# Performance work log

Hardware: AMD Instinct MI355X
Metric: run time of the kernel (lower is better)

Reference implementation:

```python
import jax, jax.numpy as jnp
import numpy as np

D_MODEL = 1024
SEQ = 2048
BATCH = 2
D_STATE = 16
D_CONV = 4
EXPAND = 2
D_INNER = EXPAND * D_MODEL          # 2048
DT_RANK = (D_MODEL + 15) // 16      # 64 (mamba_ssm default ceil(d_model/16))


def setup_inputs() -> dict:
    key = jax.random.key(0)
    keys = iter(jax.random.split(key, 40))

    def w(shape, scale):
        return jax.random.normal(next(keys), shape, jnp.float32) * scale

    inp = {"x": jax.random.normal(next(keys), (BATCH, SEQ, D_MODEL), jnp.float32)}
    inp["gamma"] = jnp.ones((D_MODEL,), jnp.float32)
    inp["beta"] = jnp.zeros((D_MODEL,), jnp.float32)
    for p in ("fw", "bw"):
        inp[f"{p}_in_w"] = w((2 * D_INNER, D_MODEL), 0.02)
        inp[f"{p}_conv_w"] = w((D_INNER, D_CONV), 0.2)
        inp[f"{p}_conv_b"] = jnp.zeros((D_INNER,), jnp.float32)
        inp[f"{p}_xproj_w"] = w((DT_RANK + 2 * D_STATE, D_INNER), 0.02)
        inp[f"{p}_dt_w"] = w((D_INNER, DT_RANK), 0.1)
        inp[f"{p}_dt_b"] = w((D_INNER,), 0.1)
        # S4D-real init: A = -[1..d_state], as in mamba_ssm
        inp[f"{p}_A_log"] = jnp.log(
            jnp.tile(jnp.arange(1, D_STATE + 1, dtype=jnp.float32), (D_INNER, 1))
        )
        inp[f"{p}_D"] = jnp.ones((D_INNER,), jnp.float32)
        inp[f"{p}_out_w"] = w((D_MODEL, D_INNER), 0.02)
    return inp


def _mamba(x, in_w, conv_w, conv_b, xproj_w, dt_w, dt_b, A_log, D_skip, out_w):
    """Single Mamba block: in_proj -> causal depthwise conv -> silu -> SSM -> gate -> out_proj."""
    B, L, _ = x.shape
    xz = x @ in_w.T                       # (B, L, 2*D_INNER)
    u, z = jnp.split(xz, 2, axis=-1)      # each (B, L, D_INNER)

    # causal depthwise conv over time
    uc = jnp.transpose(u, (0, 2, 1))      # (B, D_INNER, L)
    kernel = conv_w[:, None, :]           # (D_INNER, 1, D_CONV)
    uc = jax.lax.conv_general_dilated(
        uc, kernel, window_strides=(1,), padding=[(D_CONV - 1, 0)],
        dimension_numbers=("NCH", "OIH", "NCH"), feature_group_count=D_INNER)
    u = jax.nn.silu(jnp.transpose(uc, (0, 2, 1)) + conv_b)  # (B, L, D_INNER)

    # input-dependent dt, B, C
    dbc = u @ xproj_w.T                   # (B, L, DT_RANK + 2*D_STATE)
    dt = jax.nn.softplus(dbc[..., :DT_RANK] @ dt_w.T + dt_b)   # (B, L, D_INNER)
    Bc = dbc[..., DT_RANK:DT_RANK + D_STATE]                   # (B, L, D_STATE)
    Cc = dbc[..., DT_RANK + D_STATE:]                          # (B, L, D_STATE)
    A = -jnp.exp(A_log)                   # (D_INNER, D_STATE)

    def step(h, ins):
        dt_t, B_t, C_t, u_t = ins         # (B,Di) (B,Ds) (B,Ds) (B,Di)
        dA = jnp.exp(dt_t[..., None] * A)                      # (B, Di, Ds)
        h = dA * h + dt_t[..., None] * B_t[:, None, :] * u_t[..., None]
        y = jnp.einsum("bds,bs->bd", h, C_t)
        return h, y

    h0 = jnp.zeros((B, D_INNER, D_STATE), x.dtype)
    xs = (jnp.moveaxis(dt, 1, 0), jnp.moveaxis(Bc, 1, 0),
          jnp.moveaxis(Cc, 1, 0), jnp.moveaxis(u, 1, 0))
    _, ys = jax.lax.scan(step, h0, xs)    # ys: (L, B, D_INNER)
    y = jnp.moveaxis(ys, 0, 1) + u * D_skip
    y = y * jax.nn.silu(z)
    return y @ out_w.T                    # (B, L, D_MODEL)


def _layernorm(x, gamma, beta, eps=1e-5):
    mu = jnp.mean(x, axis=-1, keepdims=True)
    var = jnp.mean(jnp.square(x - mu), axis=-1, keepdims=True)
    return (x - mu) * jax.lax.rsqrt(var + eps) * gamma + beta


def reference(x, gamma, beta,
              fw_in_w, fw_conv_w, fw_conv_b, fw_xproj_w, fw_dt_w, fw_dt_b,
              fw_A_log, fw_D, fw_out_w,
              bw_in_w, bw_conv_w, bw_conv_b, bw_xproj_w, bw_dt_w, bw_dt_b,
              bw_A_log, bw_D, bw_out_w):
    # norm_first=True path; dropout=0 (eval)
    working = _layernorm(x, gamma, beta)
    f_out = _mamba(working, fw_in_w, fw_conv_w, fw_conv_b, fw_xproj_w,
                   fw_dt_w, fw_dt_b, fw_A_log, fw_D, fw_out_w)
    b_in = jnp.flip(working, axis=1)
    b_out = _mamba(b_in, bw_in_w, bw_conv_w, bw_conv_b, bw_xproj_w,
                   bw_dt_w, bw_dt_b, bw_A_log, bw_D, bw_out_w)
    b_out = jnp.flip(b_out, axis=1)
    return x + 0.5 * (f_out + b_out)
```

## Files before the change

### kernel.cpp

```cpp
#include <hip/hip_runtime.h>
#include <hip/hip_bf16.h>
#include <math.h>

#define B_    2
#define L_    2048
#define DM_   1024
#define DI_   2048
#define DS_   16
#define DTR_  64
#define NXZ_  4096
#define NDBC_ 96

#define NSEG   64
#define SEGLEN 32
#define CT     16
#define KS_    8
#define KO_    2

#define LOG2E 1.4426950408889634f

typedef __attribute__((ext_vector_type(8))) short bf16x8;
typedef __attribute__((ext_vector_type(4))) float f32x4;

__device__ __forceinline__ void gload_lds16(const void* g, void* l) {
    __builtin_amdgcn_global_load_lds(
        (const __attribute__((address_space(1))) void*)g,
        (__attribute__((address_space(3))) void*)l,
        16, 0, 0);
}

__device__ __forceinline__ float bf2f(short s) {
    union { unsigned u; float f; } x;
    x.u = ((unsigned)(unsigned short)s) << 16;
    return x.f;
}

__global__ __launch_bounds__(256)
void ln_kernel(const float* __restrict__ x,
               const float* __restrict__ gamma,
               const float* __restrict__ beta,
               __hip_bfloat16* __restrict__ out)
{
    int row = blockIdx.x;
    int t = threadIdx.x;
    const float* xr = x + (size_t)row * DM_;
    float4 v = ((const float4*)xr)[t];
    float s  = v.x + v.y + v.z + v.w;
    float ss = v.x*v.x + v.y*v.y + v.z*v.z + v.w*v.w;
    #pragma unroll
    for (int m = 1; m < 64; m <<= 1) {
        s  += __shfl_xor(s,  m, 64);
        ss += __shfl_xor(ss, m, 64);
    }
    __shared__ float as_[4], ass_[4];
    int w = t >> 6;
    if ((t & 63) == 0) { as_[w] = s; ass_[w] = ss; }
    __syncthreads();
    s  = as_[0] + as_[1] + as_[2] + as_[3];
    ss = ass_[0] + ass_[1] + ass_[2] + ass_[3];
    float mu  = s * (1.0f / DM_);
    float var = ss * (1.0f / DM_) - mu * mu;
    float inv = rsqrtf(var + 1e-5f);
    float4 g  = ((const float4*)gamma)[t];
    float4 bt = ((const float4*)beta)[t];
    __hip_bfloat16 ob[4];
    ob[0] = __float2bfloat16((v.x - mu) * inv * g.x + bt.x);
    ob[1] = __float2bfloat16((v.y - mu) * inv * g.y + bt.y);
    ob[2] = __float2bfloat16((v.z - mu) * inv * g.z + bt.z);
    ob[3] = __float2bfloat16((v.w - mu) * inv * g.w + bt.w);
    ((ushort4*)(out + (size_t)row * DM_))[t] = *(const ushort4*)ob;
}

__global__ __launch_bounds__(256)
void cvt_all(const float* __restrict__ inw_f, const float* __restrict__ inw_b,
             const float* __restrict__ ow_f,  const float* __restrict__ ow_b,
             const float* __restrict__ xp_f,  const float* __restrict__ xp_b,
             const float* __restrict__ dw_f,  const float* __restrict__ dw_b,
             __hip_bfloat16* __restrict__ win,
             __hip_bfloat16* __restrict__ wocat,
             __hip_bfloat16* __restrict__ xpw,
             __hip_bfloat16* __restrict__ dtw)
{
    const int N_WIN = 2 * NXZ_ * DM_;
    const int N_WO  = DM_ * NXZ_;
    const int N_XP  = 2 * NDBC_ * DI_;
    int i = (blockIdx.x * 256 + threadIdx.x) * 4;
    const float* s;
    __hip_bfloat16* dst;
    int dj;
    if (i < N_WIN) {
        int half = NXZ_ * DM_;
        s = (i < half) ? inw_f + i : inw_b + (i - half);
        dst = win; dj = i;
    } else if (i < N_WIN + N_WO) {
        int jj = i - N_WIN;
        int n = jj >> 12, c = jj & 4095;
        int dir = c >> 11, k = c & 2047;
        s = (dir ? ow_b : ow_f) + (size_t)n * DI_ + k;
        dst = wocat; dj = jj;
    } else if (i < N_WIN + N_WO + N_XP) {
        int jj = i - N_WIN - N_WO;
        int half = NDBC_ * DI_;
        s = (jj < half) ? xp_f + jj : xp_b + (jj - half);
        dst = xpw; dj = jj;
    } else {
        int jj = i - N_WIN - N_WO - N_XP;
        int half = DI_ * DTR_;
        s = (jj < half) ? dw_f + jj : dw_b + (jj - half);
        dst = dtw; dj = jj;
    }
    float4 v = *(const float4*)s;
    __hip_bfloat16 ob[4];
    ob[0] = __float2bfloat16(v.x);
    ob[1] = __float2bfloat16(v.y);
    ob[2] = __float2bfloat16(v.z);
    ob[3] = __float2bfloat16(v.w);
    *(ushort4*)(dst + dj) = *(const ushort4*)ob;
}

#define GBM 128
#define GBK 64
#define EPLD 132

template<int DBUF, int EPI>
__global__ __launch_bounds__(256)
void mfma_gemm(const __hip_bfloat16* __restrict__ A, int lda,
               const __hip_bfloat16* __restrict__ W, int ldw,
               int K, int Kslice, int Nw, int flipA,
               const float* __restrict__ aux,
               float* __restrict__ out0,
               __hip_bfloat16* __restrict__ ob1,
               __hip_bfloat16* __restrict__ ob2,
               _Float16* __restrict__ oh)
{
    __shared__ __attribute__((aligned(16))) char smem[DBUF ? 65536 : 33792];
    const int BOFF = DBUF ? 32768 : 16384;
    int t = threadIdx.x;
    int lane = t & 63, wid = t >> 6;
    int wm = wid >> 1, wn = wid & 1;

    int bx, by;
    {
        int gx = gridDim.x, gy = gridDim.y;
        int nwg = gx * gy;
        int orig = blockIdx.y * gx + blockIdx.x;
        int xcd = orig & 7;
        int c = orig >> 3;
        int npx = nwg >> 3;
        int Wc = gx < 8 ? gx : 8;
        int Hc = npx / Wc;
        int regx = gx / Wc;
        int rx = xcd % regx, ry = xcd / regx;
        bx = rx * Wc + (c % Wc);
        by = ry * Hc + (c / Wc);
    }
    int m0 = by * GBM, n0 = bx * GBM;
    int kz = blockIdx.z;
    int k_begin = kz * Kslice;
    int k_end   = (k_begin + Kslice < K) ? (k_begin + Kslice) : K;
    int ktiles  = (k_end - k_begin) / GBK;

    f32x4 acc[4][4];
    #pragma unroll
    for (int i = 0; i < 4; ++i)
        #pragma unroll
        for (int j = 0; j < 4; ++j)
            acc[i][j] = (f32x4){0.f, 0.f, 0.f, 0.f};

    int arows[4], brows[4], cbs[4];
    #pragma unroll
    for (int p = 0; p < 4; ++p) {
        int o = p * 4096 + t * 16;
        int l = o ^ (((o >> 7) & 7) << 4);
        int r = l >> 7, cb = l & 127;
        int gr = m0 + r;
        if (flipA) gr = (gr & ~(L_ - 1)) | ((L_ - 1) - (gr & (L_ - 1)));
        arows[p] = gr;
        int wr = n0 + r; if (wr >= Nw) wr = Nw - 1;
        brows[p] = wr;
        cbs[p] = cb;
    }

    #define STAGE(buf, k0)                                                        \
        {                                                                         \
            _Pragma("unroll")                                                     \
            for (int p = 0; p < 4; ++p) {                                         \
                int o = p * 4096 + t * 16;                                        \
                const char* gA = (const char*)(A + (size_t)arows[p] * lda + (k0)) \
                                 + cbs[p];                                        \
                gload_lds16(gA, smem + (buf) * 16384 + o);                        \
                const char* gB = (const char*)(W + (size_t)brows[p] * ldw + (k0)) \
                                 + cbs[p];                                        \
                gload_lds16(gB, smem + BOFF + (buf) * 16384 + o);                 \
            }                                                                     \
        }

    auto compute_tile = [&](int pbv) {
        char* bA = smem + pbv * 16384;
        char* bB = smem + BOFF + pbv * 16384;
        #pragma unroll
        for (int ks = 0; ks < 2; ++ks) {
            bf16x8 af[4], bfv[4];
            #pragma unroll
            for (int f = 0; f < 4; ++f) {
                int rowA = wm * 64 + f * 16 + (lane & 15);
                int lA = rowA * 128 + ks * 64 + ((lane >> 4) << 4);
                int pA = lA ^ ((rowA & 7) << 4);
                af[f] = *(const bf16x8*)(bA + pA);
                int rowB = wn * 64 + f * 16 + (lane & 15);
                int lB = rowB * 128 + ks * 64 + ((lane >> 4) << 4);
                int pB = lB ^ ((rowB & 7) << 4);
                bfv[f] = *(const bf16x8*)(bB + pB);
            }
            #pragma unroll
            for (int i = 0; i < 4; ++i)
                #pragma unroll
                for (int j = 0; j < 4; ++j)
                    acc[i][j] = __builtin_amdgcn_mfma_f32_16x16x32_bf16(
                        af[i], bfv[j], acc[i][j], 0, 0, 0);
        }
    };

    if (DBUF) {
        STAGE(0, k_begin);
        int pb = 0;
        for (int kt = 0; kt < ktiles; ++kt) {
            if (kt + 1 < ktiles) {
                STAGE(pb ^ 1, k_begin + (kt + 1) * GBK);
                asm volatile("s_waitcnt vmcnt(8)" ::: "memory");
            } else {
                asm volatile("s_waitcnt vmcnt(0)" ::: "memory");
            }
            __builtin_amdgcn_s_barrier();
            compute_tile(pb);
            __builtin_amdgcn_s_barrier();
            pb ^= 1;
        }
    } else {
        for (int kt = 0; kt < ktiles; ++kt) {
            STAGE(0, k_begin + kt * GBK);
            __syncthreads();
            compute_tile(0);
            __syncthreads();
        }
    }
    #undef STAGE

    if (EPI == 0) {
        bool zh = (n0 >= DI_);
        __hip_bfloat16* tile = (__hip_bfloat16*)smem;
        __syncthreads();
        #pragma unroll
        for (int i = 0; i < 4; ++i)
            #pragma unroll
            for (int j = 0; j < 4; ++j) {
                int col = wn * 64 + j * 16 + (lane & 15);
                #pragma unroll
                for (int r = 0; r < 4; ++r) {
                    int row = wm * 64 + i * 16 + ((lane >> 4) << 2) + r;
                    float v = acc[i][j][r];
                    if (zh) v = v / (1.f + __expf(-v));
                    tile[row * EPLD + col] = __float2bfloat16(v);
                }
            }
        __syncthreads();
        __hip_bfloat16* dst = zh ? ob2 : ob1;
        int nb = zh ? n0 - DI_ : n0;
        #pragma unroll
        for (int it = 0; it < 8; ++it) {
            int row = it * 16 + (t >> 4);
            int c8 = (t & 15) * 8;
            bf16x8 vv = *(const bf16x8*)&tile[row * EPLD + c8];
            *(bf16x8*)(dst + (size_t)(m0 + row) * DI_ + nb + c8) = vv;
        }
    } else if (EPI == 4) {
        _Float16* tile = (_Float16*)smem;
        float bias_j[4];
        #pragma unroll
        for (int j = 0; j < 4; ++j)
            bias_j[j] = aux[n0 + wn * 64 + j * 16 + (lane & 15)];
        __syncthreads();
        #pragma unroll
        for (int i = 0; i < 4; ++i)
            #pragma unroll
            for (int j = 0; j < 4; ++j) {
                int col = wn * 64 + j * 16 + (lane & 15);
                #pragma unroll
                for (int r = 0; r < 4; ++r) {
                    int row = wm * 64 + i * 16 + ((lane >> 4) << 2) + r;
                    float v = acc[i][j][r] + bias_j[j];
                    float sp = fmaxf(v, 0.f) + __logf(1.f + __expf(-fabsf(v)));
                    tile[row * EPLD + col] = (_Float16)sp;
                }
            }
        __syncthreads();
        #pragma unroll
        for (int it = 0; it < 8; ++it) {
            int row = it * 16 + (t >> 4);
            int c8 = (t & 15) * 8;
            bf16x8 vv = *(const bf16x8*)&tile[row * EPLD + c8];
            *(bf16x8*)(oh + (size_t)(m0 + row) * DI_ + n0 + c8) = vv;
        }
    } else if (EPI == 3) {
        __hip_bfloat16* tile = (__hip_bfloat16*)smem;
        __syncthreads();
        #pragma unroll
        for (int i = 0; i < 4; ++i)
            #pragma unroll
            for (int j = 0; j < 4; ++j) {
                int col = wn * 64 + j * 16 + (lane & 15);
                #pragma unroll
                for (int r = 0; r < 4; ++r) {
                    int row = wm * 64 + i * 16 + ((lane >> 4) << 2) + r;
                    tile[row * EPLD + col] = __float2bfloat16(acc[i][j][r]);
                }
            }
        __syncthreads();
        #pragma unroll
        for (int it = 0; it < 8; ++it) {
            int row = it * 16 + (t >> 4);
            int c8 = (t & 15) * 8;
            bf16x8 vv = *(const bf16x8*)&tile[row * EPLD + c8];
            *(bf16x8*)(ob1 + ((size_t)kz * (B_ * L_) + m0 + row) * 128 + n0 + c8) = vv;
        }
    } else {
        #pragma unroll
        for (int i = 0; i < 4; ++i) {
            #pragma unroll
            for (int j = 0; j < 4; ++j) {
                f32x4 a4 = acc[i][j];
                int gn = n0 + wn * 64 + j * 16 + (lane & 15);
                #pragma unroll
                for (int r = 0; r < 4; ++r) {
                    int gm = m0 + wm * 64 + i * 16 + ((lane >> 4) << 2) + r;
                    ob1[((size_t)kz * (B_ * L_) + gm) * DM_ + gn] =
                        __float2bfloat16(a4[r]);
                }
            }
        }
    }
}

__global__ __launch_bounds__(256)
void out_reduce(const __hip_bfloat16* __restrict__ pout,
                const float* __restrict__ x,
                float* __restrict__ out)
{
    const size_t BLDM = (size_t)B_ * L_ * DM_;
    size_t i = ((size_t)blockIdx.x * 256 + threadIdx.x) * 8;
    bf16x8 p0 = *(const bf16x8*)(pout + i);
    bf16x8 p1 = *(const bf16x8*)(pout + BLDM + i);
    float4 x0 = *(const float4*)(x + i);
    float4 x1 = *(const float4*)(x + i + 4);
    float4 o0, o1;
    o0.x = x0.x + 0.5f * (bf2f(p0[0]) + bf2f(p1[0]));
    o0.y = x0.y + 0.5f * (bf2f(p0[1]) + bf2f(p1[1]));
    o0.z = x0.z + 0.5f * (bf2f(p0[2]) + bf2f(p1[2]));
    o0.w = x0.w + 0.5f * (bf2f(p0[3]) + bf2f(p1[3]));
    o1.x = x1.x + 0.5f * (bf2f(p0[4]) + bf2f(p1[4]));
    o1.y = x1.y + 0.5f * (bf2f(p0[5]) + bf2f(p1[5]));
    o1.z = x1.z + 0.5f * (bf2f(p0[6]) + bf2f(p1[6]));
    o1.w = x1.w + 0.5f * (bf2f(p0[7]) + bf2f(p1[7]));
    *(float4*)(out + i) = o0;
    *(float4*)(out + i + 4) = o1;
}

__global__ __launch_bounds__(256)
void xproj_reduce(const __hip_bfloat16* __restrict__ pbufB,
                  float* __restrict__ dbcF,
                  __hip_bfloat16* __restrict__ dbcB)
{
    int idx = blockIdx.x * 256 + threadIdx.x;
    int m = idx >> 4;
    int n8 = (idx & 15) * 8;
    float sum[8] = {0.f,0.f,0.f,0.f,0.f,0.f,0.f,0.f};
    #pragma unroll
    for (int k = 0; k < KS_; ++k) {
        bf16x8 v = *(const bf16x8*)&pbufB[((size_t)k * (B_ * L_) + m) * 128 + n8];
        #pragma unroll
        for (int i = 0; i < 8; ++i) sum[i] += bf2f(v[i]);
    }
    #pragma unroll
    for (int i = 0; i < 8; ++i) {
        int n = n8 + i;
        if (n < NDBC_) dbcF[(size_t)m * NDBC_ + n] = sum[i];
    }
    if (n8 < DTR_) {
        short ob[8];
        #pragma unroll
        for (int i = 0; i < 8; ++i) {
            union { __hip_bfloat16 h; short s; } cv;
            cv.h = __float2bfloat16(sum[i]);
            ob[i] = cv.s;
        }
        *(bf16x8*)&dbcB[(size_t)m * DTR_ + n8] = *(const bf16x8*)ob;
    }
}

__global__ __launch_bounds__(256)
void conv_kernel(const __hip_bfloat16* __restrict__ u0,
                 const float* __restrict__ cw,
                 const float* __restrict__ cb,
                 __hip_bfloat16* __restrict__ u)
{
    int tid = blockIdx.x * 256 + threadIdx.x;
    int dcol = (tid & (DI_ / 8 - 1)) * 8;
    int r0 = (tid >> 8) * 4;
    int l0 = r0 & (L_ - 1);
    size_t base = (size_t)r0 * DI_ + dcol;

    float4 wv[8];
    float cb8[8];
    #pragma unroll
    for (int i = 0; i < 8; ++i) {
        wv[i]  = ((const float4*)cw)[dcol + i];
        cb8[i] = cb[dcol + i];
    }

    bf16x8 v[7];
    #pragma unroll
    for (int j = 0; j < 7; ++j) {
        v[j] = (bf16x8){0,0,0,0,0,0,0,0};
        if (l0 - 3 + j >= 0)
            v[j] = *(const bf16x8*)(u0 + base + (size_t)(j - 3) * DI_);
    }

    #pragma unroll
    for (int k = 0; k < 4; ++k) {
        float acc[8];
        #pragma unroll
        for (int i = 0; i < 8; ++i) acc[i] = cb8[i];
        #pragma unroll
        for (int jp = 0; jp < 4; ++jp) {
            if (l0 + k - 3 + jp >= 0) {
                bf16x8 vv = v[k + jp];
                #pragma unroll
                for (int i = 0; i < 8; ++i) {
                    float w = (jp == 0) ? wv[i].x : (jp == 1) ? wv[i].y
                              : (jp == 2) ? wv[i].z : wv[i].w;
                    acc[i] = fmaf(w, bf2f(vv[i]), acc[i]);
                }
            }
        }
        short ob[8];
        #pragma unroll
        for (int i = 0; i < 8; ++i) {
            float sv = acc[i] / (1.f + __expf(-acc[i]));
            union { __hip_bfloat16 h; short s; } cu;
            cu.h = __float2bfloat16(sv);
            ob[i] = cu.s;
        }
        *(bf16x8*)(u + base + (size_t)k * DI_) = *(const bf16x8*)ob;
    }
}


__global__ __launch_bounds__(256)
void scan_part1(const _Float16* __restrict__ dtb,
                const __hip_bfloat16* __restrict__ ub,
                const float* __restrict__ dbcF,
                const float* __restrict__ A_log,
                __hip_bfloat16* __restrict__ hseg,
                float* __restrict__ dtsum)
{
    __shared__ _Float16 sdt[CT][256];
    __shared__ __hip_bfloat16 su[CT][256];
    __shared__ float sB[CT][DS_];
    int t = threadIdx.x;
    int d0 = blockIdx.x * 256, seg = blockIdx.y, b = blockIdx.z;
    int d = d0 + t;
    size_t rowbase = (size_t)b * L_ + seg * SEGLEN;

    int rw0 = t >> 5, rw1 = 8 + (t >> 5);
    int c8 = (t & 31) * 8;
    int bl = t >> 4, bs = t & 15;

    bf16x8 vdt0 = *(const bf16x8*)&dtb[(rowbase + rw0) * DI_ + d0 + c8];
    bf16x8 vdt1 = *(const bf16x8*)&dtb[(rowbase + rw1) * DI_ + d0 + c8];
    bf16x8 vu0  = *(const bf16x8*)&ub [(rowbase + rw0) * DI_ + d0 + c8];
    bf16x8 vu1  = *(const bf16x8*)&ub [(rowbase + rw1) * DI_ + d0 + c8];
    float  vB   = dbcF[(rowbase + bl) * NDBC_ + DTR_ + bs];

    float A2[DS_], h[DS_];
    bool fastA = true;
    #pragma unroll
    for (int s = 0; s < DS_; ++s) {
        float a = __expf(A_log[d * DS_ + s]);
        A2[s] = -a * LOG2E;
        fastA = fastA && (fabsf(a - (float)(s + 1)) < 1e-3f);
        h[s] = 0.f;
    }
    float dts = 0.f;

    auto store_lds = [&]() {
        *(bf16x8*)&sdt[rw0][c8] = vdt0;
        *(bf16x8*)&sdt[rw1][c8] = vdt1;
        *(bf16x8*)&su[rw0][c8]  = vu0;
        *(bf16x8*)&su[rw1][c8]  = vu1;
        sB[bl][bs] = vB;
    };
    auto compute_chunk = [&]() {
        if (fastA) {
            for (int l = 0; l < CT; ++l) {
                float dtv = (float)sdt[l][t];
                float du  = dtv * __bfloat162float(su[l][t]);
                dts += dtv;
                float g = exp2f(-dtv * LOG2E);
                float r = 1.f;
                #pragma unroll
                for (int s = 0; s < DS_; ++s) {
                    r *= g;
                    h[s] = r * h[s] + du * sB[l][s];
                }
            }
        } else {
            for (int l = 0; l < CT; ++l) {
                float dtv = (float)sdt[l][t];
                float du  = dtv * __bfloat162float(su[l][t]);
                dts += dtv;
                #pragma unroll
                for (int s = 0; s < DS_; ++s)
                    h[s] = exp2f(dtv * A2[s]) * h[s] + du * sB[l][s];
            }
        }
    };

    store_lds();
    __syncthreads();

    vdt0 = *(const bf16x8*)&dtb[(rowbase + CT + rw0) * DI_ + d0 + c8];
    vdt1 = *(const bf16x8*)&dtb[(rowbase + CT + rw1) * DI_ + d0 + c8];
    vu0  = *(const bf16x8*)&ub [(rowbase + CT + rw0) * DI_ + d0 + c8];
    vu1  = *(const bf16x8*)&ub [(rowbase + CT + rw1) * DI_ + d0 + c8];
    vB   = dbcF[(rowbase + CT + bl) * NDBC_ + DTR_ + bs];

    compute_chunk();
    __syncthreads();
    store_lds();
    __syncthreads();
    compute_chunk();

    #pragma unroll
    for (int s = 0; s < DS_; ++s)
        hseg[(((size_t)b * NSEG + seg) * DS_ + s) * DI_ + d] =
            __float2bfloat16(h[s]);
    dtsum[((size_t)b * NSEG + seg) * DI_ + d] = dts;
}

__global__ __launch_bounds__(256)
void seg_scan(__hip_bfloat16* __restrict__ hseg,
              const float* __restrict__ dtsum,
              const float* __restrict__ A_log)
{
    int idx = blockIdx.x * 256 + threadIdx.x;
    int d = idx & (DI_ - 1);
    int s = (idx >> 11) & 15;
    int b = idx >> 15;
    float A2 = -__expf(A_log[d * DS_ + s]) * LOG2E;
    float h = 0.f;
    size_t o = (((size_t)b * NSEG + 0) * DS_ + s) * DI_ + d;
    size_t oi = ((size_t)b * NSEG + 0) * DI_ + d;
    float pv = __bfloat162float(hseg[o]), ds = dtsum[oi];
    for (int g = 0; g < NSEG; ++g) {
        float npv = 0.f, nds = 0.f;
        if (g + 1 < NSEG) {
            npv = __bfloat162float(hseg[o + (size_t)DS_ * DI_]);
            nds = dtsum[oi + DI_];
        }
        hseg[o] = __float2bfloat16(h);
        h = exp2f(A2 * ds) * h + pv;
        pv = npv; ds = nds;
        o += (size_t)DS_ * DI_;
        oi += DI_;
    }
}

__global__ __launch_bounds__(256)
void scan_part2(const _Float16* __restrict__ dtb,
                const __hip_bfloat16* __restrict__ ub,
                const __hip_bfloat16* __restrict__ zs,
                const float* __restrict__ dbcF,
                const float* __restrict__ A_log,
                const float* __restrict__ Dskip,
                const __hip_bfloat16* __restrict__ hseg,
                __hip_bfloat16* __restrict__ ycat,
                int dir)
{
    __shared__ _Float16 sdt[CT][256];
    __shared__ __hip_bfloat16 su[CT][256], sz[CT][256], sy[CT][256];
    __shared__ float sB[CT][DS_], sC[CT][DS_];
    int t = threadIdx.x;
    int d0 = blockIdx.x * 256, seg = blockIdx.y, b = blockIdx.z;
    int d = d0 + t;
    size_t rowbase = (size_t)b * L_ + seg * SEGLEN;
    int ycol0 = dir * DI_ + d0;

    int rw0 = t >> 5, rw1 = 8 + (t >> 5);
    int c8 = (t & 31) * 8;
    int bl = t >> 4, bs = t & 15;

    bf16x8 vdt0 = *(const bf16x8*)&dtb[(rowbase + rw0) * DI_ + d0 + c8];
    bf16x8 vdt1 = *(const bf16x8*)&dtb[(rowbase + rw1) * DI_ + d0 + c8];
    bf16x8 vu0  = *(const bf16x8*)&ub [(rowbase + rw0) * DI_ + d0 + c8];
    bf16x8 vu1  = *(const bf16x8*)&ub [(rowbase + rw1) * DI_ + d0 + c8];
    bf16x8 vz0  = *(const bf16x8*)&zs [(rowbase + rw0) * DI_ + d0 + c8];
    bf16x8 vz1  = *(const bf16x8*)&zs [(rowbase + rw1) * DI_ + d0 + c8];
    float  vB   = dbcF[(rowbase + bl) * NDBC_ + DTR_ + bs];
    float  vC   = dbcF[(rowbase + bl) * NDBC_ + DTR_ + DS_ + bs];

    float A2[DS_], h[DS_];
    bool fastA = true;
    #pragma unroll
    for (int s = 0; s < DS_; ++s) {
        float a = __expf(A_log[d * DS_ + s]);
        A2[s] = -a * LOG2E;
        fastA = fastA && (fabsf(a - (float)(s + 1)) < 1e-3f);
        h[s] = __bfloat162float(
            hseg[(((size_t)b * NSEG + seg) * DS_ + s) * DI_ + d]);
    }
    float Dd = Dskip[d];

    auto store_lds = [&]() {
        *(bf16x8*)&sdt[rw0][c8] = vdt0;
        *(bf16x8*)&sdt[rw1][c8] = vdt1;
        *(bf16x8*)&su[rw0][c8]  = vu0;
        *(bf16x8*)&su[rw1][c8]  = vu1;
        *(bf16x8*)&sz[rw0][c8]  = vz0;
        *(bf16x8*)&sz[rw1][c8]  = vz1;
        sB[bl][bs] = vB;
        sC[bl][bs] = vC;
    };
    auto compute_chunk = [&]() {
        if (fastA) {
            for (int l = 0; l < CT; ++l) {
                float dtv = (float)sdt[l][t];
                float uu  = __bfloat162float(su[l][t]);
                float du  = dtv * uu;
                float g = exp2f(-dtv * LOG2E);
                float r = 1.f;
                float y = 0.f;
                #pragma unroll
                for (int s = 0; s < DS_; ++s) {
                    r *= g;
                    h[s] = r * h[s] + du * sB[l][s];
                    y = fmaf(h[s], sC[l][s], y);
                }
                y = (y + Dd * uu) * __bfloat162float(sz[l][t]);
                sy[l][t] = __float2bfloat16(y);
            }
        } else {
            for (int l = 0; l < CT; ++l) {
                float dtv = (float)sdt[l][t];
                float uu  = __bfloat162float(su[l][t]);
                float du  = dtv * uu;
                float y = 0.f;
                #pragma unroll
                for (int s = 0; s < DS_; ++s) {
                    h[s] = exp2f(dtv * A2[s]) * h[s] + du * sB[l][s];
                    y = fmaf(h[s], sC[l][s], y);
                }
                y = (y + Dd * uu) * __bfloat162float(sz[l][t]);
                sy[l][t] = __float2bfloat16(y);
            }
        }
    };
    auto store_y = [&](int c) {
        #pragma unroll
        for (int p2 = 0; p2 < 2; ++p2) {
            int e = t + p2 * 256;
            int row = e >> 5, cc = (e & 31) * 8;
            int lg = seg * SEGLEN + c * CT + row;
            int lw = dir ? (L_ - 1 - lg) : lg;
            *(bf16x8*)&ycat[((size_t)b * L_ + lw) * NXZ_ + ycol0 + cc] =
                *(const bf16x8*)&sy[row][cc];
        }
    };

    store_lds();
    __syncthreads();

    vdt0 = *(const bf16x8*)&dtb[(rowbase + CT + rw0) * DI_ + d0 + c8];
    vdt1 = *(const bf16x8*)&dtb[(rowbase + CT + rw1) * DI_ + d0 + c8];
    vu0  = *(const bf16x8*)&ub [(rowbase + CT + rw0) * DI_ + d0 + c8];
    vu1  = *(const bf16x8*)&ub [(rowbase + CT + rw1) * DI_ + d0 + c8];
    vz0  = *(const bf16x8*)&zs [(rowbase + CT + rw0) * DI_ + d0 + c8];
    vz1  = *(const bf16x8*)&zs [(rowbase + CT + rw1) * DI_ + d0 + c8];
    vB   = dbcF[(rowbase + CT + bl) * NDBC_ + DTR_ + bs];
    vC   = dbcF[(rowbase + CT + bl) * NDBC_ + DTR_ + DS_ + bs];

    compute_chunk();
    __syncthreads();
    store_y(0);
    store_lds();
    __syncthreads();
    compute_chunk();
    __syncthreads();
    store_y(1);
}

extern "C" void kernel_launch(void* const* d_in, const int* in_sizes, int n_in,
                              void* d_out, int out_size, void* d_ws, size_t ws_size,
                              hipStream_t stream)
{
    (void)in_sizes; (void)n_in; (void)out_size; (void)ws_size;
    const float* x     = (const float*)d_in[0];
    const float* gamma = (const float*)d_in[1];
    const float* beta  = (const float*)d_in[2];
    float* out = (float*)d_out;

    const size_t BLDI = (size_t)B_ * L_ * DI_;

    float* ws    = (float*)d_ws;
    float* dbcF  = ws;
    float* dtsum = dbcF + (size_t)B_ * L_ * NDBC_;
    __hip_bfloat16* hsegB = (__hip_bfloat16*)(dtsum + (size_t)B_ * NSEG * DI_);
    float* shreg = (float*)(hsegB + (size_t)B_ * NSEG * DI_ * DS_);
    __hip_bfloat16* lnb  = (__hip_bfloat16*)(shreg + BLDI / 2);
    __hip_bfloat16* ub   = lnb + (size_t)B_ * L_ * DM_;
    __hip_bfloat16* zs   = ub + BLDI;
    __hip_bfloat16* ycat = zs + BLDI;
    __hip_bfloat16* win  = ycat + (size_t)B_ * L_ * NXZ_;
    __hip_bfloat16* wocat= win + (size_t)2 * NXZ_ * DM_;
    __hip_bfloat16* xpw  = wocat + (size_t)DM_ * NXZ_;
    __hip_bfloat16* dtw  = xpw + (size_t)2 * NDBC_ * DI_;
    __hip_bfloat16* dbcB = dtw + (size_t)2 * DI_ * DTR_;
    __hip_bfloat16* u0b   = (__hip_bfloat16*)shreg;
    __hip_bfloat16* pbufB = (__hip_bfloat16*)shreg;
    _Float16*       dtF   = (_Float16*)shreg;
    __hip_bfloat16* pout  = hsegB;

    dim3 blk(256);

    cvt_all<<<12928, blk, 0, stream>>>(
        (const float*)d_in[3],  (const float*)d_in[12],
        (const float*)d_in[11], (const float*)d_in[20],
        (const float*)d_in[6],  (const float*)d_in[15],
        (const float*)d_in[7],  (const float*)d_in[16],
        win, wocat, xpw, dtw);

    ln_kernel<<<B_ * L_, blk, 0, stream>>>(x, gamma, beta, lnb);

    for (int dir = 0; dir < 2; ++dir) {
        int base = 3 + dir * 9;
        const float* conv_w  = (const float*)d_in[base + 1];
        const float* conv_b  = (const float*)d_in[base + 2];
        const float* dt_b    = (const float*)d_in[base + 5];
        const float* A_log   = (const float*)d_in[base + 6];
        const float* Dsk     = (const float*)d_in[base + 7];

        mfma_gemm<1, 0><<<dim3(NXZ_ / GBM, (B_ * L_) / GBM), blk, 0, stream>>>(
            lnb, DM_, win + (size_t)dir * NXZ_ * DM_, DM_,
            DM_, DM_, NXZ_, dir, nullptr, nullptr, u0b, zs, nullptr);

        conv_kernel<<<(B_ * L_ * DI_) / 8192, blk, 0, stream>>>(
            u0b, conv_w, conv_b, ub);

        mfma_gemm<1, 3><<<dim3(1, (B_ * L_) / GBM, KS_), blk, 0, stream>>>(
            ub, DI_, xpw + (size_t)dir * NDBC_ * DI_, DI_,
            DI_, DI_ / KS_, NDBC_, 0, nullptr, nullptr, pbufB, nullptr, nullptr);
        xproj_reduce<<<(B_ * L_ * 16) / 256, blk, 0, stream>>>(pbufB, dbcF, dbcB);

        mfma_gemm<0, 4><<<dim3(DI_ / GBM, (B_ * L_) / GBM), blk, 0, stream>>>(
            dbcB, DTR_, dtw + (size_t)dir * DI_ * DTR_, DTR_,
            DTR_, DTR_, DI_, 0, dt_b, nullptr, nullptr, nullptr, dtF);

        scan_part1<<<dim3(DI_ / 256, NSEG, B_), blk, 0, stream>>>(
            dtF, ub, dbcF, A_log, hsegB, dtsum);
        seg_scan<<<(B_ * DI_ * DS_) / 256, blk, 0, stream>>>(hsegB, dtsum, A_log);
        scan_part2<<<dim3(DI_ / 256, NSEG, B_), blk, 0, stream>>>(
            dtF, ub, zs, dbcF, A_log, Dsk, hsegB, ycat, dir);
    }

    mfma_gemm<1, 1><<<dim3(DM_ / GBM, (B_ * L_) / GBM, KO_), blk, 0, stream>>>(
        ycat, NXZ_, wocat, NXZ_, NXZ_, NXZ_ / KO_, DM_, 0,
        nullptr, nullptr, pout, nullptr, nullptr);
    out_reduce<<<(B_ * L_ * DM_) / 2048, blk, 0, stream>>>(pout, x, out);
}
```

Baseline: 329.6 us.

## Use dedicated 256x256-tile in-projection GEMM with XCD-aware block remapping

Replaces the generic 128x128 MFMA GEMM for the in-projection with a dedicated kernel using 256x256 tiles, 512 threads and 128KB of dynamic LDS with double buffering. Block indices are remapped so neighbouring tiles land on the same XCD for better L2 reuse. The aim is fewer loads per FLOP and better cache locality. The trade-offs are only 16x16=256 workgroups, so under one wave across the CUs, and high register pressure from 32 accumulators per thread.

```diff
diff --git a/kernel.cpp b/kernel.cpp
--- a/kernel.cpp
+++ b/kernel.cpp
@@ -118,6 +118,151 @@
     *(ushort4*)(dst + dj) = *(const ushort4*)ob;
 }
 
+#define EP2LD 260
+
+__global__ __launch_bounds__(512, 2)
+void inproj_gemm256(const __hip_bfloat16* __restrict__ A,
+                    const __hip_bfloat16* __restrict__ W,
+                    int flipA,
+                    __hip_bfloat16* __restrict__ ob1,
+                    __hip_bfloat16* __restrict__ ob2)
+{
+    extern __shared__ __attribute__((aligned(16))) char smem[];
+    const int BOFF = 65536;
+    int t = threadIdx.x;
+    int lane = t & 63, wid = t >> 6;
+    int wm = wid >> 2, wn = wid & 3;
+
+    int bx, by;
+    {
+        int gx = gridDim.x, gy = gridDim.y;
+        int nwg = gx * gy;
+        int orig = blockIdx.y * gx + blockIdx.x;
+        int xcd = orig & 7;
+        int c = orig >> 3;
+        int npx = nwg >> 3;
+        int Wc = gx < 8 ? gx : 8;
+        int Hc = npx / Wc;
+        int regx = gx / Wc;
+        int rx = xcd % regx, ry = xcd / regx;
+        bx = rx * Wc + (c % Wc);
+        by = ry * Hc + (c / Wc);
+    }
+    int m0 = by * 256, n0 = bx * 256;
+
+    f32x4 acc[8][4];
+    #pragma unroll
+    for (int i = 0; i < 8; ++i)
+        #pragma unroll
+        for (int j = 0; j < 4; ++j)
+            acc[i][j] = (f32x4){0.f, 0.f, 0.f, 0.f};
+
+    int arows[4], brows[4], cbs[4];
+    #pragma unroll
+    for (int p = 0; p < 4; ++p) {
+        int o = p * 8192 + t * 16;
+        int l = o ^ (((o >> 7) & 7) << 4);
+        int r = l >> 7, cb = l & 127;
+        int gr = m0 + r;
+        if (flipA) gr = (gr & ~(L_ - 1)) | ((L_ - 1) - (gr & (L_ - 1)));
+        arows[p] = gr;
+        brows[p] = n0 + r;
+        cbs[p] = cb;
+    }
+
+    #define STAGE2(buf, k0)                                                       \
+        {                                                                         \
+            _Pragma("unroll")                                                     \
+            for (int p = 0; p < 4; ++p) {                                         \
+                int o = p * 8192 + t * 16;                                        \
+                const char* gA = (const char*)(A + (size_t)arows[p] * DM_ + (k0)) \
+                                 + cbs[p];                                        \
+                gload_lds16(gA, smem + (buf) * 32768 + o);                        \
+                const char* gB = (const char*)(W + (size_t)brows[p] * DM_ + (k0)) \
+                                 + cbs[p];                                        \
+                gload_lds16(gB, smem + BOFF + (buf) * 32768 + o);                 \
+            }                                                                     \
+        }
+
+    auto compute_tile = [&](int pbv) {
+        char* bA = smem + pbv * 32768;
+        char* bB = smem + BOFF + pbv * 32768;
+        #pragma unroll
+        for (int ks = 0; ks < 2; ++ks) {
+            bf16x8 af[8], bfv[4];
+            #pragma unroll
+            for (int f = 0; f < 8; ++f) {
+                int rowA = wm * 128 + f * 16 + (lane & 15);
+                int lA = rowA * 128 + ks * 64 + ((lane >> 4) << 4);
+                int pA = lA ^ ((rowA & 7) << 4);
+                af[f] = *(const bf16x8*)(bA + pA);
+            }
+            #pragma unroll
+            for (int j = 0; j < 4; ++j) {
+                int rowB = wn * 64 + j * 16 + (lane & 15);
+                int lB = rowB * 128 + ks * 64 + ((lane >> 4) << 4);
+                int pB = lB ^ ((rowB & 7) << 4);
+                bfv[j] = *(const bf16x8*)(bB + pB);
+            }
+            #pragma unroll
+            for (int i = 0; i < 8; ++i)
+                #pragma unroll
+                for (int j = 0; j < 4; ++j)
+                    acc[i][j] = __builtin_amdgcn_mfma_f32_16x16x32_bf16(
+                        af[i], bfv[j], acc[i][j], 0, 0, 0);
+        }
+    };
+
+    const int ktiles = DM_ / 64;
+    STAGE2(0, 0);
+    int pb = 0;
+    for (int kt = 0; kt < ktiles; ++kt) {
+        if (kt + 1 < ktiles) {
+            STAGE2(pb ^ 1, (kt + 1) * 64);
+            asm volatile("s_waitcnt vmcnt(8)" ::: "memory");
+        } else {
+            asm volatile("s_waitcnt vmcnt(0)" ::: "memory");
+        }
+        __builtin_amdgcn_s_barrier();
+        compute_tile(pb);
+        __builtin_amdgcn_s_barrier();
+        pb ^= 1;
+    }
+    #undef STAGE2
+
+    bool zh = (n0 >= DI_);
+    __hip_bfloat16* dst = zh ? ob2 : ob1;
+    int nb = zh ? n0 - DI_ : n0;
+    __hip_bfloat16* tile = (__hip_bfloat16*)smem;
+    #pragma unroll
+    for (int h = 0; h < 2; ++h) {
+        __syncthreads();
+        if (wm == h) {
+            #pragma unroll
+            for (int f = 0; f < 8; ++f)
+                #pragma unroll
+                for (int j = 0; j < 4; ++j) {
+                    int col = wn * 64 + j * 16 + (lane & 15);
+                    #pragma unroll
+                    for (int r = 0; r < 4; ++r) {
+                        int rowl = f * 16 + ((lane >> 4) << 2) + r;
+                        float v = acc[f][j][r];
+                        if (zh) v = v / (1.f + __expf(-v));
+                        tile[rowl * EP2LD + col] = __float2bfloat16(v);
+                    }
+                }
+        }
+        __syncthreads();
+        #pragma unroll
+        for (int it = 0; it < 8; ++it) {
+            int row = it * 16 + (t >> 5);
+            int c8 = (t & 31) * 8;
+            bf16x8 vv = *(const bf16x8*)&tile[row * EP2LD + c8];
+            *(bf16x8*)(dst + (size_t)(m0 + h * 128 + row) * DI_ + nb + c8) = vv;
+        }
+    }
+}
+
 #define GBM 128
 #define GBK 64
 #define EPLD 132
@@ -748,9 +893,8 @@
         const float* A_log   = (const float*)d_in[base + 6];
         const float* Dsk     = (const float*)d_in[base + 7];
 
-        mfma_gemm<1, 0><<<dim3(NXZ_ / GBM, (B_ * L_) / GBM), blk, 0, stream>>>(
-            lnb, DM_, win + (size_t)dir * NXZ_ * DM_, DM_,
-            DM_, DM_, NXZ_, dir, nullptr, nullptr, u0b, zs, nullptr);
+        inproj_gemm256<<<dim3(NXZ_ / 256, (B_ * L_) / 256), 512, 131072, stream>>>(
+            lnb, win + (size_t)dir * NXZ_ * DM_, dir, u0b, zs);
 
         conv_kernel<<<(B_ * L_ * DI_) / 8192, blk, 0, stream>>>(
             u0b, conv_w, conv_b, ub);
```

After: 445.1 us. 35.0% more time.
